# Kernel optimization log

Measured on AMD Instinct MI355X. Metric: run time of the kernel, lower is better.

## Reference

```python
import jax, jax.numpy as jnp
import numpy as np
from jax import lax

BETA = 0.1
N_CLUSTERS = 64


def setup_inputs() -> dict:
    key = jax.random.key(0)
    ks = jax.random.split(key, 10)
    L, B, Hin, H = 200, 2048, 64, 256
    s = lambda k, shape, scale=0.05: jax.random.normal(k, shape, dtype=jnp.float32) * scale
    return {
        "X": jax.random.normal(ks[0], (L, B, Hin), dtype=jnp.float32),
        "W_ih0": s(ks[1], (4 * H, Hin)),
        "W_hh0": s(ks[2], (4 * H, H)),
        "b_ih0": s(ks[3], (4 * H,)),
        "b_hh0": s(ks[4], (4 * H,)),
        "W_ih1": s(ks[5], (4 * H, H)),
        "W_hh1": s(ks[6], (4 * H, H)),
        "b_ih1": s(ks[7], (4 * H,)),
        "b_hh1": s(ks[8], (4 * H,)),
        "clusters": jax.random.normal(ks[9], (N_CLUSTERS, H), dtype=jnp.float32),
    }


def _lstm_layer(x, W_ih, W_hh, b_ih, b_hh):
    # x: (L, B, I) -> outputs (L, B, H); torch gate order i, f, g, o
    H = W_hh.shape[1]
    B = x.shape[1]
    b = b_ih + b_hh

    def step(carry, xt):
        h, c = carry
        gates = xt @ W_ih.T + h @ W_hh.T + b  # (B, 4H)
        i, f, g, o = jnp.split(gates, 4, axis=-1)
        c = jax.nn.sigmoid(f) * c + jax.nn.sigmoid(i) * jnp.tanh(g)
        h = jax.nn.sigmoid(o) * jnp.tanh(c)
        return (h, c), h

    h0 = jnp.zeros((B, H), x.dtype)
    (_, _), ys = lax.scan(step, (h0, h0), x)
    return ys


def _encode(X, W_ih0, W_hh0, b_ih0, b_hh0, W_ih1, W_hh1, b_ih1, b_hh1):
    y0 = _lstm_layer(X, W_ih0, W_hh0, b_ih0, b_hh0)
    y1 = _lstm_layer(y0, W_ih1, W_hh1, b_ih1, b_hh1)
    return y1[-1]  # latent_X: (B, H), last timestep of top layer


def reference(X, W_ih0, W_hh0, b_ih0, b_hh0, W_ih1, W_hh1, b_ih1, b_hh1, clusters):
    latent_X = _encode(X, W_ih0, W_hh0, b_ih0, b_hh0, W_ih1, W_hh1, b_ih1, b_hh1)

    # kmeans assignment on detached latents (l2 distance)
    lat_sg = lax.stop_gradient(latent_X)
    d2 = (jnp.sum(lat_sg * lat_sg, -1, keepdims=True)
          - 2.0 * lat_sg @ clusters.T
          + jnp.sum(clusters * clusters, -1))  # (B, K)
    cluster_id = jnp.argmin(d2, axis=-1)  # (B,)

    # centroid update from assigned (detached) points; keep old centroid if empty
    sums = jax.ops.segment_sum(lat_sg, cluster_id, num_segments=N_CLUSTERS)
    counts = jax.ops.segment_sum(jnp.ones((lat_sg.shape[0],), lat_sg.dtype),
                                 cluster_id, num_segments=N_CLUSTERS)
    upd = jnp.where(counts[:, None] > 0, sums / jnp.maximum(counts, 1.0)[:, None], clusters)

    # vectorized per-sample cluster distance loss: sum_i 0.5*beta*||latent_i - c[id_i]||^2
    diff = latent_X - upd[cluster_id]  # gather (B, H)
    dist_loss = 0.5 * BETA * jnp.sum(diff * diff)
    return latent_X, dist_loss
```

## Files before the change

kernel.cpp:

```cpp
#include <hip/hip_runtime.h>
#include <hip/hip_bf16.h>
#include <math.h>

typedef unsigned short u16;
typedef __attribute__((ext_vector_type(8))) __bf16 bf16x8;
typedef __attribute__((ext_vector_type(4))) float f32x4;

#define LSTM_L 200
#define LSTM_B 2048
#define LSTM_HIN 64
#define LSTM_H 256
#define NCLUST 64
#define HALF_BETA 0.05f

__device__ __forceinline__ void gload_lds16(const void* g, void* l) {
    __builtin_amdgcn_global_load_lds(
        (__attribute__((address_space(1))) void*)g,
        (__attribute__((address_space(3))) void*)l, 16, 0, 0);
}

template<int KIN>
__global__ __launch_bounds__(256) void pack_weights(
    const float* __restrict__ Wih, const float* __restrict__ Whh,
    u16* __restrict__ Wcat)
{
    constexpr int KTOT = KIN + LSTM_H;
    const int total = 1024 * KTOT;
    for (int i = blockIdx.x * 256 + threadIdx.x; i < total; i += gridDim.x * 256) {
        const int j = i / KTOT;
        const int k = i - j * KTOT;
        const float v = (k < KIN) ? Wih[(size_t)j * KIN + k]
                                  : Whh[(size_t)j * LSTM_H + (k - KIN)];
        const __bf16 b = (__bf16)v;
        Wcat[i] = __builtin_bit_cast(u16, b);
    }
}

template<int KIN, bool XF32>
__device__ __forceinline__ void run_layer(
    const void* __restrict__ xsrc,
    const u16* __restrict__ hin,
    const u16* __restrict__ Wcat,
    const float* __restrict__ bih, const float* __restrict__ bhh,
    u16* __restrict__ hout,
    float* __restrict__ latout,
    float* __restrict__ cst,
    int blk, u16* As, u16* Bs, int tid)
{
    constexpr int KTOT = KIN + LSTM_H;
    constexpr int NCH = KTOT / 32;
    const int lane = tid & 63;
    const int w = tid >> 6;
    const int b0 = (blk & 15) * 128;
    const int n0 = (blk >> 4) * 16;

    f32x4 acc[2][4];
#pragma unroll
    for (int i = 0; i < 2; ++i)
#pragma unroll
        for (int j = 0; j < 4; ++j) acc[i][j] = f32x4{0.f, 0.f, 0.f, 0.f};

    for (int ch = 0; ch < NCH; ++ch) {
        const int k0 = ch * 32;
        if (XF32 && k0 < KIN) {
            const float* xs = (const float*)xsrc;
#pragma unroll
            for (int p = 0; p < 2; ++p) {
                const int slot = p * 256 + tid;
                const int row = slot >> 2;
                const int kk = (slot & 3) * 8;
                const float* s = xs + (size_t)(b0 + row) * KIN + k0 + kk;
                const float4 v0 = *(const float4*)s;
                const float4 v1 = *(const float4*)(s + 4);
                bf16x8 pk;
                pk[0] = (__bf16)v0.x; pk[1] = (__bf16)v0.y;
                pk[2] = (__bf16)v0.z; pk[3] = (__bf16)v0.w;
                pk[4] = (__bf16)v1.x; pk[5] = (__bf16)v1.y;
                pk[6] = (__bf16)v1.z; pk[7] = (__bf16)v1.w;
                *(bf16x8*)&As[slot * 8] = pk;
            }
        } else {
            const u16* src; int stride, kk;
            if (!XF32 && k0 < KIN) { src = (const u16*)xsrc; stride = KIN; kk = k0; }
            else                   { src = hin; stride = LSTM_H; kk = k0 - KIN; }
#pragma unroll
            for (int p = 0; p < 2; ++p) {
                const int slot = p * 256 + tid;
                const int row = slot >> 2;
                const int c16 = slot & 3;
                gload_lds16(src + (size_t)(b0 + row) * stride + kk + c16 * 8,
                            &As[slot * 8]);
            }
        }
        {
            const int slot = tid;
            const int row = slot >> 2;
            const int c16 = slot & 3;
            const int j = (row >> 4) * 256 + n0 + (row & 15);
            gload_lds16(Wcat + (size_t)j * KTOT + k0 + c16 * 8, &Bs[slot * 8]);
        }
        __syncthreads();

        bf16x8 af[2], bf_[4];
#pragma unroll
        for (int fm = 0; fm < 2; ++fm)
            af[fm] = *(const bf16x8*)&As[(w * 32 + fm * 16 + (lane & 15)) * 32 +
                                         (lane >> 4) * 8];
#pragma unroll
        for (int fn = 0; fn < 4; ++fn)
            bf_[fn] = *(const bf16x8*)&Bs[(fn * 16 + (lane & 15)) * 32 +
                                          (lane >> 4) * 8];
#pragma unroll
        for (int fm = 0; fm < 2; ++fm)
#pragma unroll
            for (int fn = 0; fn < 4; ++fn)
                acc[fm][fn] = __builtin_amdgcn_mfma_f32_16x16x32_bf16(
                    af[fm], bf_[fn], acc[fm][fn], 0, 0, 0);
        __syncthreads();
    }

    const int n = n0 + (lane & 15);
    const float bi = bih[n]       + bhh[n];
    const float bff = bih[n + 256] + bhh[n + 256];
    const float bg = bih[n + 512] + bhh[n + 512];
    const float bo = bih[n + 768] + bhh[n + 768];
#pragma unroll
    for (int fm = 0; fm < 2; ++fm) {
#pragma unroll
        for (int r = 0; r < 4; ++r) {
            const int m = b0 + w * 32 + fm * 16 + (lane >> 4) * 4 + r;
            const size_t idx = (size_t)m * LSTM_H + n;
            const float gi = acc[fm][0][r] + bi;
            const float gf = acc[fm][1][r] + bff;
            const float gg = acc[fm][2][r] + bg;
            const float go = acc[fm][3][r] + bo;
            const float si = 1.f / (1.f + expf(-gi));
            const float sf = 1.f / (1.f + expf(-gf));
            const float so = 1.f / (1.f + expf(-go));
            const float cn = sf * cst[idx] + si * tanhf(gg);
            cst[idx] = cn;
            const float hv = so * tanhf(cn);
            const __bf16 hb = (__bf16)hv;
            hout[idx] = __builtin_bit_cast(u16, hb);
            if (latout) latout[idx] = hv;
        }
    }
}

__global__ __launch_bounds__(256) void lstm_step2(
    const float* __restrict__ xt,
    const u16* __restrict__ h0in, u16* __restrict__ h0out, float* __restrict__ c0,
    const u16* __restrict__ Wc0, const float* __restrict__ bih0, const float* __restrict__ bhh0,
    const u16* __restrict__ h1in, u16* __restrict__ h1out, float* __restrict__ c1,
    const u16* __restrict__ Wc1, const float* __restrict__ bih1, const float* __restrict__ bhh1,
    float* __restrict__ latout, int do0, int do1)
{
    __shared__ u16 As[128 * 32];
    __shared__ u16 Bs[64 * 32];
    const int tid = threadIdx.x;
    if (blockIdx.x < 256) {
        if (do0)
            run_layer<LSTM_HIN, true>(xt, h0in, Wc0, bih0, bhh0, h0out, nullptr,
                                      c0, blockIdx.x, As, Bs, tid);
    } else {
        if (do1)
            run_layer<LSTM_H, false>(h0in, h1in, Wc1, bih1, bhh1, h1out, latout,
                                     c1, blockIdx.x - 256, As, Bs, tid);
    }
}

__global__ __launch_bounds__(64) void assign_kernel(
    const float* __restrict__ lat, const float* __restrict__ clusters,
    int* __restrict__ ids)
{
    __shared__ float row[LSTM_H];
    const int b = blockIdx.x;
    const int k = threadIdx.x;
    for (int i = k; i < LSTM_H; i += 64) row[i] = lat[(size_t)b * LSTM_H + i];
    __syncthreads();
    const float* ck = clusters + (size_t)k * LSTM_H;
    float d = 0.f;
#pragma unroll 8
    for (int i = 0; i < LSTM_H; ++i) { const float t = row[i] - ck[i]; d += t * t; }
    int idx = k;
    for (int off = 32; off > 0; off >>= 1) {
        const float od = __shfl_down(d, off, 64);
        const int   oi = __shfl_down(idx, off, 64);
        if (od < d || (od == d && oi < idx)) { d = od; idx = oi; }
    }
    if (k == 0) ids[b] = idx;
}

__global__ __launch_bounds__(256) void centroid_kernel(
    const float* __restrict__ lat, const int* __restrict__ ids,
    const float* __restrict__ clusters, float* __restrict__ upd)
{
    const int k = blockIdx.x;
    const int h = threadIdx.x;
    float s = 0.f;
    int cnt = 0;
    for (int b = 0; b < LSTM_B; ++b) {
        if (ids[b] == k) { s += lat[(size_t)b * LSTM_H + h]; cnt++; }
    }
    upd[(size_t)k * LSTM_H + h] =
        (cnt > 0) ? s / (float)cnt : clusters[(size_t)k * LSTM_H + h];
}

__global__ __launch_bounds__(256) void loss_kernel(
    const float* __restrict__ lat, const int* __restrict__ ids,
    const float* __restrict__ upd, float* __restrict__ out_loss)
{
    float p = 0.f;
    const int total = LSTM_B * LSTM_H;
    for (int idx = blockIdx.x * blockDim.x + threadIdx.x; idx < total;
         idx += gridDim.x * blockDim.x) {
        const int b = idx >> 8;
        const float d = lat[idx] - upd[(size_t)ids[b] * LSTM_H + (idx & 255)];
        p += d * d;
    }
    for (int off = 32; off > 0; off >>= 1) p += __shfl_down(p, off, 64);
    __shared__ float wsum[4];
    const int lane = threadIdx.x & 63, wid = threadIdx.x >> 6;
    if (lane == 0) wsum[wid] = p;
    __syncthreads();
    if (threadIdx.x == 0)
        atomicAdd(out_loss, HALF_BETA * (wsum[0] + wsum[1] + wsum[2] + wsum[3]));
}

extern "C" void kernel_launch(void* const* d_in, const int* in_sizes, int n_in,
                              void* d_out, int out_size, void* d_ws, size_t ws_size,
                              hipStream_t stream)
{
    const float* X     = (const float*)d_in[0];
    const float* Wih0  = (const float*)d_in[1];
    const float* Whh0  = (const float*)d_in[2];
    const float* bih0  = (const float*)d_in[3];
    const float* bhh0  = (const float*)d_in[4];
    const float* Wih1  = (const float*)d_in[5];
    const float* Whh1  = (const float*)d_in[6];
    const float* bih1  = (const float*)d_in[7];
    const float* bhh1  = (const float*)d_in[8];
    const float* clust = (const float*)d_in[9];

    float* out = (float*)d_out;
    char* base = (char*)d_ws;

    const size_t MB = 1u << 20;
    float* c0  = (float*)(base + 0 * MB);
    float* c1  = (float*)(base + 2 * MB);
    u16* h0a   = (u16*)(base + 4 * MB);
    u16* h0b   = (u16*)(base + 5 * MB);
    u16* h1a   = (u16*)(base + 6 * MB);
    u16* h1b   = (u16*)(base + 7 * MB);
    u16* Wc0   = (u16*)(base + 8 * MB);
    u16* Wc1   = (u16*)(base + 9 * MB);
    float* upd = (float*)(base + 10 * MB);
    int* ids   = (int*)(base + 10 * MB + 256 * 1024);

    const size_t BH = (size_t)LSTM_B * LSTM_H;

    hipMemsetAsync(c0, 0, 4 * MB, stream);
    hipMemsetAsync(h0a, 0, MB, stream);
    hipMemsetAsync(h1a, 0, MB, stream);
    hipMemsetAsync(out + BH, 0, sizeof(float), stream);

    pack_weights<LSTM_HIN><<<320, 256, 0, stream>>>(Wih0, Whh0, Wc0);
    pack_weights<LSTM_H>  <<<512, 256, 0, stream>>>(Wih1, Whh1, Wc1);

    u16* h0cur = h0a; u16* h0nxt = h0b;
    u16* h1cur = h1a; u16* h1nxt = h1b;
    for (int s = 0; s <= LSTM_L; ++s) {
        const int do0 = (s < LSTM_L) ? 1 : 0;
        const int do1 = (s > 0) ? 1 : 0;
        const float* xt = do0 ? X + (size_t)s * LSTM_B * LSTM_HIN : nullptr;
        float* lat = (s == LSTM_L) ? out : nullptr;
        lstm_step2<<<512, 256, 0, stream>>>(
            xt, h0cur, h0nxt, c0, Wc0, bih0, bhh0,
            h1cur, h1nxt, c1, Wc1, bih1, bhh1, lat, do0, do1);
        if (do0) { u16* t = h0cur; h0cur = h0nxt; h0nxt = t; }
        if (do1) { u16* t = h1cur; h1cur = h1nxt; h1nxt = t; }
    }

    assign_kernel<<<LSTM_B, 64, 0, stream>>>(out, clust, ids);
    centroid_kernel<<<NCLUST, 256, 0, stream>>>(out, ids, clust, upd);
    loss_kernel<<<256, 256, 0, stream>>>(out, ids, upd, out + BH);
}
```

Baseline: 3.003 ms.

## Hold LSTM weights in registers and stage full h-tile in swizzled LDS

Weights are pre-packed into MFMA fragment order so each wave loads its B operands once into registers per step, instead of streaming them through LDS every K-chunk. The whole A tile (x and h rows) is staged into a 128KB XOR-swizzled LDS buffer with a single barrier, removing per-chunk syncs. Gate columns are interleaved so paired lanes exchange gates via shuffle, with fast rcp/exp activations. Also caches cluster ids in shared memory for the centroid kernel. The trade-offs are high register pressure from the register-held weights (spill risk), larger blocks with fewer of them, and slightly lower activation precision.

```diff
diff --git a/kernel.cpp b/kernel.cpp
--- a/kernel.cpp
+++ b/kernel.cpp
@@ -12,160 +12,213 @@
 #define LSTM_H 256
 #define NCLUST 64
 #define HALF_BETA 0.05f
+#define LDS_BYTES 131072
 
 __device__ __forceinline__ void gload_lds16(const void* g, void* l) {
     __builtin_amdgcn_global_load_lds(
-        (__attribute__((address_space(1))) void*)g,
+        (__attribute__((address_space(1))) const void*)g,
         (__attribute__((address_space(3))) void*)l, 16, 0, 0);
 }
 
+__device__ __forceinline__ float fast_sigmoid(float x) {
+    return __builtin_amdgcn_rcpf(1.f + __expf(-x));
+}
+__device__ __forceinline__ float fast_tanh(float x) {
+    return 2.f * __builtin_amdgcn_rcpf(1.f + __expf(-2.f * x)) - 1.f;
+}
+
 template<int KIN>
-__global__ __launch_bounds__(256) void pack_weights(
+__global__ __launch_bounds__(256) void pack_frag(
     const float* __restrict__ Wih, const float* __restrict__ Whh,
-    u16* __restrict__ Wcat)
-{
-    constexpr int KTOT = KIN + LSTM_H;
-    const int total = 1024 * KTOT;
+    u16* __restrict__ Wp)
+{
+    constexpr int NCH = (KIN + LSTM_H) / 32;
+    const int total = 1024 * (KIN + LSTM_H);
     for (int i = blockIdx.x * 256 + threadIdx.x; i < total; i += gridDim.x * 256) {
-        const int j = i / KTOT;
-        const int k = i - j * KTOT;
+        const int e = i & 7;
+        int t = i >> 3;
+        const int lane = t & 63; t >>= 6;
+        const int nf = t & 1;    t >>= 1;
+        const int ch = t % NCH;  t /= NCH;
+        const int wn = t & 3;
+        const int nb = t >> 2;
+        const int l15 = lane & 15;
+        const int j = (2 * nf + (l15 & 1)) * 256 + nb * 32 + wn * 8 + (l15 >> 1);
+        const int k = ch * 32 + ((lane >> 4) << 3) + e;
         const float v = (k < KIN) ? Wih[(size_t)j * KIN + k]
                                   : Whh[(size_t)j * LSTM_H + (k - KIN)];
-        const __bf16 b = (__bf16)v;
-        Wcat[i] = __builtin_bit_cast(u16, b);
-    }
-}
-
-template<int KIN, bool XF32>
+        Wp[i] = __builtin_bit_cast(u16, (__bf16)v);
+    }
+}
+
+template<int KIN>
 __device__ __forceinline__ void run_layer(
-    const void* __restrict__ xsrc,
-    const u16* __restrict__ hin,
-    const u16* __restrict__ Wcat,
+    const float* __restrict__ xf32,
+    const u16* __restrict__ hbelow,
+    const u16* __restrict__ hself,
+    const u16* __restrict__ Wp,
     const float* __restrict__ bih, const float* __restrict__ bhh,
-    u16* __restrict__ hout,
-    float* __restrict__ latout,
+    u16* __restrict__ hout, float* __restrict__ latout,
     float* __restrict__ cst,
-    int blk, u16* As, u16* Bs, int tid)
-{
-    constexpr int KTOT = KIN + LSTM_H;
-    constexpr int NCH = KTOT / 32;
+    int blk, char* smem, int tid)
+{
+    constexpr int NCH = (KIN + LSTM_H) / 32;
+    constexpr bool IS_L0 = (KIN == 64);
     const int lane = tid & 63;
     const int w = tid >> 6;
-    const int b0 = (blk & 15) * 128;
-    const int n0 = (blk >> 4) * 16;
-
-    f32x4 acc[2][4];
-#pragma unroll
-    for (int i = 0; i < 2; ++i)
-#pragma unroll
-        for (int j = 0; j < 4; ++j) acc[i][j] = f32x4{0.f, 0.f, 0.f, 0.f};
-
+    const int wm = w >> 2;
+    const int wn = w & 3;
+    const int l15 = lane & 15;
+    const int q = lane >> 4;
+    const int mb = blk >> 3;
+    const int nb = blk & 7;
+    const int b0 = mb * 128;
+
+    bf16x8 Breg[NCH][2];
+    {
+        const u16* wp = Wp + (size_t)((nb * 4 + wn) * NCH) * 1024 + lane * 8;
+#pragma unroll
+        for (int ch = 0; ch < NCH; ++ch)
+#pragma unroll
+            for (int nf = 0; nf < 2; ++nf)
+                Breg[ch][nf] = *(const bf16x8*)(wp + (ch * 2 + nf) * 512);
+    }
+
+    const int hcol = nb * 32 + wn * 8 + (l15 >> 1);
+    const int rowA = wm * 64;
+    float cp[4][4];
+#pragma unroll
+    for (int mf = 0; mf < 4; ++mf)
+#pragma unroll
+        for (int r = 0; r < 4; ++r)
+            cp[mf][r] = cst[(size_t)(b0 + rowA + mf * 16 + q * 4 + r) * 256 + hcol];
+
+    const int gpar = l15 & 1;
+    const float b0a = bih[gpar * 256 + hcol] + bhh[gpar * 256 + hcol];
+    const float b1a = bih[(2 + gpar) * 256 + hcol] + bhh[(2 + gpar) * 256 + hcol];
+
+    if (IS_L0) {
+#pragma unroll
+        for (int i = 0; i < 8; ++i) {
+            const int slot = i * 512 + tid;
+            const int row = slot >> 5;
+            const int so = (slot & 31) * 16;
+            const int koff = so ^ ((row & 7) << 4);
+            gload_lds16((const char*)hself + (size_t)(b0 + row) * 512 + koff,
+                        smem + slot * 16);
+        }
+#pragma unroll
+        for (int p = 0; p < 2; ++p) {
+            const int slot = p * 512 + tid;
+            const int row = slot >> 3;
+            const int so = (slot & 7) * 16;
+            const int koff = so ^ ((row & 7) << 4);
+            const float* s = xf32 + (size_t)(b0 + row) * 64 + (koff >> 1);
+            const float4 v0 = *(const float4*)s;
+            const float4 v1 = *(const float4*)(s + 4);
+            bf16x8 pk;
+            pk[0] = (__bf16)v0.x; pk[1] = (__bf16)v0.y;
+            pk[2] = (__bf16)v0.z; pk[3] = (__bf16)v0.w;
+            pk[4] = (__bf16)v1.x; pk[5] = (__bf16)v1.y;
+            pk[6] = (__bf16)v1.z; pk[7] = (__bf16)v1.w;
+            *(bf16x8*)(smem + 65536 + slot * 16) = pk;
+        }
+    } else {
+#pragma unroll
+        for (int i = 0; i < 16; ++i) {
+            const int slot = i * 512 + tid;
+            const int row = slot >> 6;
+            const int so = (slot & 63) * 16;
+            const int koff = so ^ ((row & 7) << 4);
+            const char* src = (koff < 512)
+                ? (const char*)hbelow + (size_t)(b0 + row) * 512 + koff
+                : (const char*)hself + (size_t)(b0 + row) * 512 + (koff - 512);
+            gload_lds16(src, smem + slot * 16);
+        }
+    }
+    __syncthreads();
+
+    f32x4 acc[4][2];
+#pragma unroll
+    for (int mf = 0; mf < 4; ++mf)
+#pragma unroll
+        for (int nf = 0; nf < 2; ++nf) acc[mf][nf] = f32x4{0.f, 0.f, 0.f, 0.f};
+
+    const int qoff = q * 16;
+    const int swzl = (l15 & 7) << 4;
+#pragma unroll
     for (int ch = 0; ch < NCH; ++ch) {
-        const int k0 = ch * 32;
-        if (XF32 && k0 < KIN) {
-            const float* xs = (const float*)xsrc;
-#pragma unroll
-            for (int p = 0; p < 2; ++p) {
-                const int slot = p * 256 + tid;
-                const int row = slot >> 2;
-                const int kk = (slot & 3) * 8;
-                const float* s = xs + (size_t)(b0 + row) * KIN + k0 + kk;
-                const float4 v0 = *(const float4*)s;
-                const float4 v1 = *(const float4*)(s + 4);
-                bf16x8 pk;
-                pk[0] = (__bf16)v0.x; pk[1] = (__bf16)v0.y;
-                pk[2] = (__bf16)v0.z; pk[3] = (__bf16)v0.w;
-                pk[4] = (__bf16)v1.x; pk[5] = (__bf16)v1.y;
-                pk[6] = (__bf16)v1.z; pk[7] = (__bf16)v1.w;
-                *(bf16x8*)&As[slot * 8] = pk;
+        bf16x8 af[4];
+#pragma unroll
+        for (int mf = 0; mf < 4; ++mf) {
+            const int row = rowA + mf * 16 + l15;
+            const char* ap;
+            if (IS_L0) {
+                if (ch < 2)
+                    ap = smem + 65536 + row * 128 + ((ch * 64 + qoff) ^ swzl);
+                else
+                    ap = smem + row * 512 + (((ch - 2) * 64 + qoff) ^ swzl);
+            } else {
+                ap = smem + row * 1024 + ((ch * 64 + qoff) ^ swzl);
             }
-        } else {
-            const u16* src; int stride, kk;
-            if (!XF32 && k0 < KIN) { src = (const u16*)xsrc; stride = KIN; kk = k0; }
-            else                   { src = hin; stride = LSTM_H; kk = k0 - KIN; }
-#pragma unroll
-            for (int p = 0; p < 2; ++p) {
-                const int slot = p * 256 + tid;
-                const int row = slot >> 2;
-                const int c16 = slot & 3;
-                gload_lds16(src + (size_t)(b0 + row) * stride + kk + c16 * 8,
-                            &As[slot * 8]);
+            af[mf] = *(const bf16x8*)ap;
+        }
+#pragma unroll
+        for (int mf = 0; mf < 4; ++mf)
+#pragma unroll
+            for (int nf = 0; nf < 2; ++nf)
+                acc[mf][nf] = __builtin_amdgcn_mfma_f32_16x16x32_bf16(
+                    af[mf], Breg[ch][nf], acc[mf][nf], 0, 0, 0);
+    }
+
+#pragma unroll
+    for (int mf = 0; mf < 4; ++mf) {
+#pragma unroll
+        for (int r = 0; r < 4; ++r) {
+            const float a0 = acc[mf][0][r] + b0a;
+            const float a1 = acc[mf][1][r] + b1a;
+            const float p0 = __shfl_xor(a0, 1);
+            const float p1 = __shfl_xor(a1, 1);
+            const float gi = gpar ? p0 : a0;
+            const float gf = gpar ? a0 : p0;
+            const float gg = gpar ? p1 : a1;
+            const float go = gpar ? a1 : p1;
+            const float cn = fast_sigmoid(gf) * cp[mf][r]
+                           + fast_sigmoid(gi) * fast_tanh(gg);
+            const float hv = fast_sigmoid(go) * fast_tanh(cn);
+            const size_t oidx =
+                (size_t)(b0 + rowA + mf * 16 + q * 4 + r) * 256 + hcol;
+            if (gpar) {
+                cst[oidx] = cn;
+            } else if (latout) {
+                latout[oidx] = hv;
+            } else {
+                hout[oidx] = __builtin_bit_cast(u16, (__bf16)hv);
             }
         }
-        {
-            const int slot = tid;
-            const int row = slot >> 2;
-            const int c16 = slot & 3;
-            const int j = (row >> 4) * 256 + n0 + (row & 15);
-            gload_lds16(Wcat + (size_t)j * KTOT + k0 + c16 * 8, &Bs[slot * 8]);
-        }
-        __syncthreads();
-
-        bf16x8 af[2], bf_[4];
-#pragma unroll
-        for (int fm = 0; fm < 2; ++fm)
-            af[fm] = *(const bf16x8*)&As[(w * 32 + fm * 16 + (lane & 15)) * 32 +
-                                         (lane >> 4) * 8];
-#pragma unroll
-        for (int fn = 0; fn < 4; ++fn)
-            bf_[fn] = *(const bf16x8*)&Bs[(fn * 16 + (lane & 15)) * 32 +
-                                          (lane >> 4) * 8];
-#pragma unroll
-        for (int fm = 0; fm < 2; ++fm)
-#pragma unroll
-            for (int fn = 0; fn < 4; ++fn)
-                acc[fm][fn] = __builtin_amdgcn_mfma_f32_16x16x32_bf16(
-                    af[fm], bf_[fn], acc[fm][fn], 0, 0, 0);
-        __syncthreads();
-    }
-
-    const int n = n0 + (lane & 15);
-    const float bi = bih[n]       + bhh[n];
-    const float bff = bih[n + 256] + bhh[n + 256];
-    const float bg = bih[n + 512] + bhh[n + 512];
-    const float bo = bih[n + 768] + bhh[n + 768];
-#pragma unroll
-    for (int fm = 0; fm < 2; ++fm) {
-#pragma unroll
-        for (int r = 0; r < 4; ++r) {
-            const int m = b0 + w * 32 + fm * 16 + (lane >> 4) * 4 + r;
-            const size_t idx = (size_t)m * LSTM_H + n;
-            const float gi = acc[fm][0][r] + bi;
-            const float gf = acc[fm][1][r] + bff;
-            const float gg = acc[fm][2][r] + bg;
-            const float go = acc[fm][3][r] + bo;
-            const float si = 1.f / (1.f + expf(-gi));
-            const float sf = 1.f / (1.f + expf(-gf));
-            const float so = 1.f / (1.f + expf(-go));
-            const float cn = sf * cst[idx] + si * tanhf(gg);
-            cst[idx] = cn;
-            const float hv = so * tanhf(cn);
-            const __bf16 hb = (__bf16)hv;
-            hout[idx] = __builtin_bit_cast(u16, hb);
-            if (latout) latout[idx] = hv;
-        }
-    }
-}
-
-__global__ __launch_bounds__(256) void lstm_step2(
+    }
+}
+
+__global__ __launch_bounds__(512, 2) void lstm_slot(
     const float* __restrict__ xt,
-    const u16* __restrict__ h0in, u16* __restrict__ h0out, float* __restrict__ c0,
-    const u16* __restrict__ Wc0, const float* __restrict__ bih0, const float* __restrict__ bhh0,
-    const u16* __restrict__ h1in, u16* __restrict__ h1out, float* __restrict__ c1,
-    const u16* __restrict__ Wc1, const float* __restrict__ bih1, const float* __restrict__ bhh1,
+    const u16* __restrict__ h0c, u16* __restrict__ h0n, float* __restrict__ c0,
+    const u16* __restrict__ Wp0,
+    const float* __restrict__ bih0, const float* __restrict__ bhh0,
+    const u16* __restrict__ h1c, u16* __restrict__ h1n, float* __restrict__ c1,
+    const u16* __restrict__ Wp1,
+    const float* __restrict__ bih1, const float* __restrict__ bhh1,
     float* __restrict__ latout, int do0, int do1)
 {
-    __shared__ u16 As[128 * 32];
-    __shared__ u16 Bs[64 * 32];
+    extern __shared__ char smem[];
     const int tid = threadIdx.x;
-    if (blockIdx.x < 256) {
+    if (blockIdx.x < 128) {
         if (do0)
-            run_layer<LSTM_HIN, true>(xt, h0in, Wc0, bih0, bhh0, h0out, nullptr,
-                                      c0, blockIdx.x, As, Bs, tid);
+            run_layer<LSTM_HIN>(xt, nullptr, h0c, Wp0, bih0, bhh0,
+                                h0n, nullptr, c0, blockIdx.x, smem, tid);
     } else {
         if (do1)
-            run_layer<LSTM_H, false>(h0in, h1in, Wc1, bih1, bhh1, h1out, latout,
-                                     c1, blockIdx.x - 256, As, Bs, tid);
+            run_layer<LSTM_H>(nullptr, h0c, h1c, Wp1, bih1, bhh1,
+                              h1n, latout, c1, blockIdx.x - 128, smem, tid);
     }
 }
 
@@ -195,12 +248,15 @@
     const float* __restrict__ lat, const int* __restrict__ ids,
     const float* __restrict__ clusters, float* __restrict__ upd)
 {
+    __shared__ int sid[LSTM_B];
     const int k = blockIdx.x;
     const int h = threadIdx.x;
+    for (int i = threadIdx.x; i < LSTM_B; i += 256) sid[i] = ids[i];
+    __syncthreads();
     float s = 0.f;
     int cnt = 0;
     for (int b = 0; b < LSTM_B; ++b) {
-        if (ids[b] == k) { s += lat[(size_t)b * LSTM_H + h]; cnt++; }
+        if (sid[b] == k) { s += lat[(size_t)b * LSTM_H + h]; cnt++; }
     }
     upd[(size_t)k * LSTM_H + h] =
         (cnt > 0) ? s / (float)cnt : clusters[(size_t)k * LSTM_H + h];
@@ -244,41 +300,44 @@
 
     float* out = (float*)d_out;
     char* base = (char*)d_ws;
-
     const size_t MB = 1u << 20;
-    float* c0  = (float*)(base + 0 * MB);
-    float* c1  = (float*)(base + 2 * MB);
-    u16* h0a   = (u16*)(base + 4 * MB);
-    u16* h0b   = (u16*)(base + 5 * MB);
-    u16* h1a   = (u16*)(base + 6 * MB);
-    u16* h1b   = (u16*)(base + 7 * MB);
-    u16* Wc0   = (u16*)(base + 8 * MB);
-    u16* Wc1   = (u16*)(base + 9 * MB);
+
+    u16* Wp0   = (u16*)(base + 0 * MB);
+    u16* Wp1   = (u16*)(base + 1 * MB);
+    u16* h0a   = (u16*)(base + 2 * MB);
+    u16* h0b   = (u16*)(base + 3 * MB);
+    u16* h1a   = (u16*)(base + 4 * MB);
+    u16* h1b   = (u16*)(base + 5 * MB);
+    float* c0  = (float*)(base + 6 * MB);
+    float* c1  = (float*)(base + 8 * MB);
     float* upd = (float*)(base + 10 * MB);
     int* ids   = (int*)(base + 10 * MB + 256 * 1024);
 
     const size_t BH = (size_t)LSTM_B * LSTM_H;
 
-    hipMemsetAsync(c0, 0, 4 * MB, stream);
     hipMemsetAsync(h0a, 0, MB, stream);
     hipMemsetAsync(h1a, 0, MB, stream);
+    hipMemsetAsync(c0, 0, 4 * MB, stream);
     hipMemsetAsync(out + BH, 0, sizeof(float), stream);
 
-    pack_weights<LSTM_HIN><<<320, 256, 0, stream>>>(Wih0, Whh0, Wc0);
-    pack_weights<LSTM_H>  <<<512, 256, 0, stream>>>(Wih1, Whh1, Wc1);
-
-    u16* h0cur = h0a; u16* h0nxt = h0b;
-    u16* h1cur = h1a; u16* h1nxt = h1b;
+    pack_frag<LSTM_HIN><<<320, 256, 0, stream>>>(Wih0, Whh0, Wp0);
+    pack_frag<LSTM_H>  <<<512, 256, 0, stream>>>(Wih1, Whh1, Wp1);
+
+    hipFuncSetAttribute((const void*)lstm_slot,
+                        hipFuncAttributeMaxDynamicSharedMemorySize, LDS_BYTES);
+
+    u16* h0c = h0a; u16* h0n = h0b;
+    u16* h1c = h1a; u16* h1n = h1b;
     for (int s = 0; s <= LSTM_L; ++s) {
         const int do0 = (s < LSTM_L) ? 1 : 0;
         const int do1 = (s > 0) ? 1 : 0;
         const float* xt = do0 ? X + (size_t)s * LSTM_B * LSTM_HIN : nullptr;
         float* lat = (s == LSTM_L) ? out : nullptr;
-        lstm_step2<<<512, 256, 0, stream>>>(
-            xt, h0cur, h0nxt, c0, Wc0, bih0, bhh0,
-            h1cur, h1nxt, c1, Wc1, bih1, bhh1, lat, do0, do1);
-        if (do0) { u16* t = h0cur; h0cur = h0nxt; h0nxt = t; }
-        if (do1) { u16* t = h1cur; h1cur = h1nxt; h1nxt = t; }
+        lstm_slot<<<256, 512, LDS_BYTES, stream>>>(
+            xt, h0c, h0n, c0, Wp0, bih0, bhh0,
+            h1c, h1n, c1, Wp1, bih1, bhh1, lat, do0, do1);
+        if (do0) { u16* t = h0c; h0c = h0n; h0n = t; }
+        if (do1) { u16* t = h1c; h1c = h1n; h1n = t; }
     }
 
     assign_kernel<<<LSTM_B, 64, 0, stream>>>(out, clust, ids);
```

Measured after the change: 3.184 ms. +6.1%, slower.
